# Performance work log

Measured on AMD Instinct MI355X. Metric: run time of the kernel, lower is better.

Reference implementation:

```python
import jax, jax.numpy as jnp
import numpy as np

KAPPA = 1.0
SIGMA = 0.3
EPS = 1e-5  # torch BatchNorm1d default eps


def _bn(y, g, b):
    # training-mode batch norm: biased batch statistics over the batch axis
    mu = jnp.mean(y, axis=0)
    var = jnp.mean((y - mu) ** 2, axis=0)
    return g * (y - mu) * jax.lax.rsqrt(var + EPS) + b


def _hid(x, W, b, g, be):
    # Linear -> BatchNorm1d -> ReLU
    return jax.nn.relu(_bn(x @ W + b, g, be))


def setup_inputs() -> dict:
    key = jax.random.key(0)
    ks = jax.random.split(key, 12)
    B, D, H, T = 2048, 256, 266, 51  # H = dim + 10
    S = T - 1
    sc = jnp.float32(0.1)
    f32 = jnp.float32
    inp = {}
    inp["x"] = jax.random.normal(ks[0], (B, D), f32)
    inp["dW"] = jax.random.normal(ks[1], (S, B, D), f32)   # hoisted per-step noise xi
    inp["law"] = jax.random.normal(ks[2], (S, D), f32)
    inp["timegrid"] = jnp.linspace(0.0, 1.0, T).astype(f32)
    # per-timestep MLP stacks (i_h1 / h1_h2 / h2_o)
    inp["W1"] = sc * jax.random.normal(ks[3], (S, D, H), f32)
    inp["b1"] = jnp.zeros((S, H), f32)
    inp["g1"] = jnp.ones((S, H), f32)
    inp["be1"] = jnp.zeros((S, H), f32)
    inp["W2"] = sc * jax.random.normal(ks[4], (S, H, H), f32)
    inp["b2"] = jnp.zeros((S, H), f32)
    inp["g2"] = jnp.ones((S, H), f32)
    inp["be2"] = jnp.zeros((S, H), f32)
    inp["W3"] = sc * jax.random.normal(ks[5], (S, H, D), f32)
    inp["b3"] = jnp.zeros((S, D), f32)
    # v0 network (v0_i_h1 / v0_h1_h2 / v0_h2_o, all Linear+BN+ReLU)
    inp["Wv1"] = sc * jax.random.normal(ks[6], (D, H), f32)
    inp["bv1"] = jnp.zeros((H,), f32)
    inp["gv1"] = jnp.ones((H,), f32)
    inp["bev1"] = jnp.zeros((H,), f32)
    inp["Wv2"] = sc * jax.random.normal(ks[7], (H, H), f32)
    inp["bv2"] = jnp.zeros((H,), f32)
    inp["gv2"] = jnp.ones((H,), f32)
    inp["bev2"] = jnp.zeros((H,), f32)
    inp["Wv3"] = sc * jax.random.normal(ks[8], (H, 1), f32)
    inp["bv3"] = jnp.zeros((1,), f32)
    inp["gv3"] = jnp.ones((1,), f32)
    inp["bev3"] = jnp.zeros((1,), f32)
    return inp


def reference(x, dW, law, timegrid,
              W1, b1, g1, be1, W2, b2, g2, be2, W3, b3,
              Wv1, bv1, gv1, bev1, Wv2, bv2, gv2, bev2, Wv3, bv3, gv3, bev3):
    hgrid = jnp.diff(timegrid)  # [S]
    # v0 network evaluated on the initial state (note: last stage is also Linear+BN+ReLU)
    v0 = _hid(_hid(_hid(x, Wv1, bv1, gv1, bev1), Wv2, bv2, gv2, bev2), Wv3, bv3, gv3, bev3)  # [B,1]

    def step(carry, xs):
        xc, v = carry
        w1, bb1, gg1, bbe1, w2, bb2, gg2, bbe2, w3, bb3, li, dw, h = xs
        h1 = _hid(xc, w1, bb1, gg1, bbe1)
        h2 = _hid(h1, w2, bb2, gg2, bbe2)
        grad = h2 @ w3 + bb3                                   # [B,D]
        # f = kappa^2/2 * ||x - law_i||^2 + 1/2 * ||alpha||^2,  alpha = -grad
        f = 0.5 * KAPPA ** 2 * jnp.sum((xc - li) ** 2, axis=1) + 0.5 * jnp.sum(grad ** 2, axis=1)
        noise = SIGMA * jnp.sqrt(h) * dw                       # [B,D]
        # diag(grad @ noise^T) == rowwise dot product: O(B*D) instead of O(B^2*D)
        v = v - (f * h)[:, None] + jnp.sum(grad * noise, axis=1, keepdims=True)
        xc = xc - grad * h + noise
        return (xc, v), None

    (x_final, v), _ = jax.lax.scan(
        step, (x, v0),
        (W1, b1, g1, be1, W2, b2, g2, be2, W3, b3, law, dW, hgrid))
    return v  # [B,1]; (x_final and the path are byproducts of the same scan)
```

## Files before the change

kernel.cpp:

```cpp
#include <hip/hip_runtime.h>
#include <hip/hip_bf16.h>


#define BATCH 2048
#define DD    256
#define HH    266
#define HP    272
#define SS    50
#define BN_EPS 1e-5f
#define SIG   0.3f
#define AS_STRIDE 296

#define XC_OFF 0
#define Y1_OFF 524288
#define Y2_OFF 1081344
#define V_OFF  1638400
#define S1_OFF 1640448
#define S2_OFF 1649152
#define S1V_OFF 1657856
#define S2V_OFF 1662208
#define SV_OFF  1666560
#define WQ_OFF  1666576

#define W1S 69632
#define W2S 78336
#define W3S 73728
#define W1Q_OFF 0
#define W2Q_OFF 3481600
#define W3Q_OFF 7398400
#define WV1Q_OFF 11084800
#define WV2Q_OFF 11154432

#define BAR_OFF 7283200

typedef unsigned short ushort_t;
using short8 = __attribute__((ext_vector_type(8))) short;
using f32x4  = __attribute__((ext_vector_type(4))) float;

__device__ __forceinline__ ushort_t f2b(float f) {
    unsigned u = __float_as_uint(f);
    unsigned r = u + 0x7FFF + ((u >> 16) & 1);
    return (ushort_t)(r >> 16);
}

__device__ __forceinline__ float ld_coh(const float* p) {
    return __hip_atomic_load((const float*)p, __ATOMIC_RELAXED, __HIP_MEMORY_SCOPE_AGENT);
}

__device__ __forceinline__ void prefetch16(const void* p, int n16, int tid) {
    const f32x4* q = (const f32x4*)p;
    for (int i = tid; i < n16; i += 512) {
        f32x4 t = q[i];
        asm volatile("" :: "v"(t));
    }
}

__global__ __launch_bounds__(256) void k_conv(const float* __restrict__ src,
                                              ushort_t* __restrict__ dst,
                                              int K, int N, int KT, int NT,
                                              long total) {
    long t = (long)blockIdx.x * 256 + threadIdx.x;
    if (t >= total) return;
    int per = KT * NT * 512;
    int step = (int)(t / per);
    int e = (int)(t - (long)step * per);
    int kt = e / (NT * 512);
    int r = e - kt * NT * 512;
    int nt = r / 512;
    int r2 = r & 511;
    int lane = r2 >> 3;
    int j = r2 & 7;
    int k = kt * 32 + (lane >> 4) * 8 + j;
    int n = nt * 16 + (lane & 15);
    float v = (k < K && n < N) ? src[(size_t)step * K * N + (size_t)k * N + n] : 0.f;
    dst[t] = f2b(v);
}

__global__ __launch_bounds__(256) void k_pre(float* __restrict__ ws) {
    unsigned* bar = (unsigned*)(ws + BAR_OFF);
    for (int i = threadIdx.x; i < 512; i += 256) atomicExch(bar + i, 0u);
}

__device__ __forceinline__ void grid_bar(unsigned* bar, unsigned gen, int bid) {
    __syncthreads();
    if (threadIdx.x == 0) {
        unsigned* leaf = bar + (bid & 7) * 32;
        unsigned* root = bar + 256;
        unsigned* rel  = bar + 288;
        bool done = false;
        unsigned a = __hip_atomic_fetch_add(leaf, 1u, __ATOMIC_RELAXED, __HIP_MEMORY_SCOPE_AGENT);
        if (a == gen * 16u + 15u) {
            unsigned r = __hip_atomic_fetch_add(root, 1u, __ATOMIC_RELAXED, __HIP_MEMORY_SCOPE_AGENT);
            if (r == gen * 8u + 7u) {
                __hip_atomic_store(rel, gen + 1u, __ATOMIC_RELAXED, __HIP_MEMORY_SCOPE_AGENT);
                done = true;
            }
        }
        if (!done) {
            while (__hip_atomic_load(rel, __ATOMIC_RELAXED, __HIP_MEMORY_SCOPE_AGENT) < gen + 1u)
                __builtin_amdgcn_s_sleep(1);
        }
        asm volatile("" ::: "memory");
    }
    __syncthreads();
}

__device__ __forceinline__ void compute_ac_coh(const float* __restrict__ si,
                                               const float* __restrict__ g,
                                               const float* __restrict__ be,
                                               float (*AC)[HP]) {
    int t = threadIdx.x;
    if (t < HP) {
        float a = 0.f, c = 0.f;
        if (t < HH) {
            float s = 0.f, q = 0.f;
            #pragma unroll
            for (int r = 0; r < 8; ++r) {
                s += ld_coh(si + r * 544 + t);
                q += ld_coh(si + r * 544 + 272 + t);
            }
            float mu  = s * (1.0f / 2048.0f);
            float var = q * (1.0f / 2048.0f) - mu * mu;
            float rs  = rsqrtf(fmaxf(var, 0.0f) + BN_EPS);
            a = g[t] * rs;
            c = be[t] - mu * a;
        }
        AC[0][t] = a;
        AC[1][t] = c;
    }
}

__device__ __forceinline__ void dev_lin16(
    int bid, int mode, int KT,
    const float* __restrict__ gsrc,
    const float* __restrict__ lsrc,
    const float* __restrict__ stats_in, const float* __restrict__ g,
    const float* __restrict__ be,
    const ushort_t* __restrict__ Wq, const float* __restrict__ bias,
    float* __restrict__ ylds,
    float* __restrict__ stats_out,
    float* __restrict__ zero_ptr,
    ushort_t* __restrict__ As, float (*AC)[HP])
{
    const int tid  = threadIdx.x;
    const int lane = tid & 63;
    const int wv   = tid >> 6;
    const int quad = lane >> 4;
    const int l15  = lane & 15;
    const int row0 = bid * 16;

    if (zero_ptr != nullptr) {
        int z = bid * 512 + tid;
        if (z < 4352) atomicExch(zero_ptr + z, 0.0f);
    }

    if (mode == 2) { compute_ac_coh(stats_in, g, be, AC); __syncthreads(); }

    const int PAIRS = KT * 16;
    for (int idx = tid; idx < 16 * PAIRS; idx += 512) {
        int m  = idx / PAIRS;
        int kk = (idx - m * PAIRS) * 2;
        float v0, v1;
        if (mode == 2) {
            v0 = (kk < HH)   ? fmaxf(fmaf(AC[0][kk],   lsrc[m * HP + kk],   AC[1][kk]),   0.f) : 0.f;
            v1 = (kk+1 < HH) ? fmaxf(fmaf(AC[0][kk+1], lsrc[m * HP + kk+1], AC[1][kk+1]), 0.f) : 0.f;
        } else {
            v0 = gsrc[(size_t)(row0 + m) * DD + kk];
            v1 = gsrc[(size_t)(row0 + m) * DD + kk + 1];
        }
        ((unsigned int*)As)[m * (AS_STRIDE/2) + (kk >> 1)] =
            (unsigned int)f2b(v0) | ((unsigned int)f2b(v1) << 16);
    }
    __syncthreads();

    f32x4 acc[3];
    #pragma unroll
    for (int i = 0; i < 3; ++i) acc[i] = (f32x4){0.f, 0.f, 0.f, 0.f};

    for (int kt = 0; kt < KT; ++kt) {
        short8 af = *(const short8*)(&As[l15 * AS_STRIDE + kt * 32 + quad * 8]);
        const ushort_t* wp = Wq + ((size_t)(kt * 17 + wv)) * 512 + lane * 8;
        #pragma unroll
        for (int i = 0; i < 3; ++i) {
            if (i < 2 || wv == 0) {
                short8 bf = *(const short8*)(wp + (size_t)i * 8 * 512);
                acc[i] = __builtin_amdgcn_mfma_f32_16x16x32_bf16(af, bf, acc[i], 0, 0, 0);
            }
        }
    }

    #pragma unroll
    for (int i = 0; i < 3; ++i) {
        if (i == 2 && wv != 0) continue;
        int t = wv + 8 * i;
        int col = t * 16 + l15;
        float bj = (col < HH) ? bias[col] : 0.f;
        float y0 = acc[i][0] + bj, y1 = acc[i][1] + bj;
        float y2 = acc[i][2] + bj, y3 = acc[i][3] + bj;
        ylds[(quad*4 + 0) * HP + col] = y0;
        ylds[(quad*4 + 1) * HP + col] = y1;
        ylds[(quad*4 + 2) * HP + col] = y2;
        ylds[(quad*4 + 3) * HP + col] = y3;
        float sp = y0 + y1 + y2 + y3;
        float sq = y0*y0 + y1*y1 + y2*y2 + y3*y3;
        sp += __shfl_xor(sp, 16); sp += __shfl_xor(sp, 32);
        sq += __shfl_xor(sq, 16); sq += __shfl_xor(sq, 32);
        if (quad == 0 && col < HH) {
            float* spp = stats_out + (bid & 7) * 544;
            atomicAdd(spp + col, sp);
            atomicAdd(spp + 272 + col, sq);
        }
    }
}

__device__ __forceinline__ void dev_fused16(
    int bid,
    const float* __restrict__ y2l,
    const float* __restrict__ stats_in,
    const float* __restrict__ g2, const float* __restrict__ be2,
    const ushort_t* __restrict__ W3q, const float* __restrict__ b3,
    const float* __restrict__ law, const float* __restrict__ dWs,
    const float* __restrict__ tg, int s, int doP1,
    float* __restrict__ xcl,
    float* __restrict__ vv, float* __restrict__ outv,
    const ushort_t* __restrict__ W1q, const float* __restrict__ b1n,
    float* __restrict__ y1l,
    float* __restrict__ stats_out,
    float* __restrict__ zero_ptr,
    ushort_t* __restrict__ As, float (*AC)[HP], float* __restrict__ red)
{
    const int tid  = threadIdx.x;
    const int lane = tid & 63;
    const int wv   = tid >> 6;
    const int quad = lane >> 4;
    const int l15  = lane & 15;
    const int row0 = bid * 16;

    if (zero_ptr != nullptr) {
        int z = bid * 512 + tid;
        if (z < 4352) atomicExch(zero_ptr + z, 0.0f);
    }

    compute_ac_coh(stats_in, g2, be2, AC);
    __syncthreads();

    for (int idx = tid; idx < 16 * 144; idx += 512) {
        int m  = idx / 144;
        int kk = (idx - m * 144) * 2;
        float v0 = (kk < HH)   ? fmaxf(fmaf(AC[0][kk],   y2l[m * HP + kk],   AC[1][kk]),   0.f) : 0.f;
        float v1 = (kk+1 < HH) ? fmaxf(fmaf(AC[0][kk+1], y2l[m * HP + kk+1], AC[1][kk+1]), 0.f) : 0.f;
        ((unsigned int*)As)[m * (AS_STRIDE/2) + (kk >> 1)] =
            (unsigned int)f2b(v0) | ((unsigned int)f2b(v1) << 16);
    }
    __syncthreads();

    f32x4 acc[2];
    acc[0] = (f32x4){0.f,0.f,0.f,0.f};
    acc[1] = (f32x4){0.f,0.f,0.f,0.f};
    for (int kt = 0; kt < 9; ++kt) {
        short8 af = *(const short8*)(&As[l15 * AS_STRIDE + kt * 32 + quad * 8]);
        const ushort_t* wp = W3q + ((size_t)(kt * 16 + wv)) * 512 + lane * 8;
        acc[0] = __builtin_amdgcn_mfma_f32_16x16x32_bf16(af, *(const short8*)(wp),           acc[0], 0, 0, 0);
        acc[1] = __builtin_amdgcn_mfma_f32_16x16x32_bf16(af, *(const short8*)(wp + 8 * 512), acc[1], 0, 0, 0);
    }

    const float h   = tg[s + 1] - tg[s];
    const float srt = SIG * sqrtf(h);
    float grad[2][4], xcv[2][4], dwv[2][4];
    float sxr[4] = {0,0,0,0}, sgr[4] = {0,0,0,0}, sgnr[4] = {0,0,0,0};
    #pragma unroll
    for (int i = 0; i < 2; ++i) {
        int col = (wv + 8*i) * 16 + l15;
        #pragma unroll
        for (int r = 0; r < 4; ++r) {
            int rl = quad * 4 + r;
            float gd = acc[i][r] + b3[col];
            float xv = xcl[rl * DD + col];
            float dw = dWs[(size_t)(row0 + rl) * DD + col];
            float d  = xv - law[col];
            grad[i][r] = gd; xcv[i][r] = xv; dwv[i][r] = dw;
            sxr[r]  = fmaf(d, d, sxr[r]);
            sgr[r]  = fmaf(gd, gd, sgr[r]);
            sgnr[r] = fmaf(gd, dw, sgnr[r]);
        }
    }
    #pragma unroll
    for (int off = 1; off < 16; off <<= 1) {
        #pragma unroll
        for (int r = 0; r < 4; ++r) {
            sxr[r]  += __shfl_xor(sxr[r],  off);
            sgr[r]  += __shfl_xor(sgr[r],  off);
            sgnr[r] += __shfl_xor(sgnr[r], off);
        }
    }
    if (l15 == 0) {
        #pragma unroll
        for (int r = 0; r < 4; ++r) {
            int rr = quad * 4 + r;
            red[(wv * 16 + rr) * 3 + 0] = sxr[r];
            red[(wv * 16 + rr) * 3 + 1] = sgr[r];
            red[(wv * 16 + rr) * 3 + 2] = sgnr[r];
        }
    }
    __syncthreads();

    if (tid < 16) {
        float sx = 0.f, sg = 0.f, sgn = 0.f;
        #pragma unroll
        for (int w = 0; w < 8; ++w) {
            sx  += red[(w * 16 + tid) * 3 + 0];
            sg  += red[(w * 16 + tid) * 3 + 1];
            sgn += red[(w * 16 + tid) * 3 + 2];
        }
        int row = row0 + tid;
        float f  = 0.5f * (sx + sg);
        float vn = vv[row] - f * h + srt * sgn;
        vv[row] = vn;
        if (s == SS - 1) outv[row] = vn;
    }

    #pragma unroll
    for (int i = 0; i < 2; ++i) {
        int col = (wv + 8*i) * 16 + l15;
        #pragma unroll
        for (int r = 0; r < 4; ++r) {
            int rl = quad * 4 + r;
            float xn = xcv[i][r] - grad[i][r] * h + srt * dwv[i][r];
            xcl[rl * DD + col] = xn;
            if (doP1) As[rl * AS_STRIDE + col] = f2b(xn);
        }
    }
    if (!doP1) return;
    __syncthreads();

    f32x4 acc2[3];
    #pragma unroll
    for (int i = 0; i < 3; ++i) acc2[i] = (f32x4){0.f, 0.f, 0.f, 0.f};
    for (int kt = 0; kt < 8; ++kt) {
        short8 af = *(const short8*)(&As[l15 * AS_STRIDE + kt * 32 + quad * 8]);
        const ushort_t* wp = W1q + ((size_t)(kt * 17 + wv)) * 512 + lane * 8;
        #pragma unroll
        for (int i = 0; i < 3; ++i) {
            if (i < 2 || wv == 0) {
                short8 bf = *(const short8*)(wp + (size_t)i * 8 * 512);
                acc2[i] = __builtin_amdgcn_mfma_f32_16x16x32_bf16(af, bf, acc2[i], 0, 0, 0);
            }
        }
    }
    #pragma unroll
    for (int i = 0; i < 3; ++i) {
        if (i == 2 && wv != 0) continue;
        int t = wv + 8 * i;
        int col = t * 16 + l15;
        float bj = (col < HH) ? b1n[col] : 0.f;
        float y0 = acc2[i][0] + bj, y1 = acc2[i][1] + bj;
        float y2 = acc2[i][2] + bj, y3 = acc2[i][3] + bj;
        y1l[(quad*4 + 0) * HP + col] = y0;
        y1l[(quad*4 + 1) * HP + col] = y1;
        y1l[(quad*4 + 2) * HP + col] = y2;
        y1l[(quad*4 + 3) * HP + col] = y3;
        float sp = y0 + y1 + y2 + y3;
        float sq = y0*y0 + y1*y1 + y2*y2 + y3*y3;
        sp += __shfl_xor(sp, 16); sp += __shfl_xor(sp, 32);
        sq += __shfl_xor(sq, 16); sq += __shfl_xor(sq, 32);
        if (quad == 0 && col < HH) {
            float* spp = stats_out + (bid & 7) * 544;
            atomicAdd(spp + col, sp);
            atomicAdd(spp + 272 + col, sq);
        }
    }
}

__device__ __forceinline__ void dev_v0l3_16(
    int bid, const float* __restrict__ y2l, const float* __restrict__ stats_in,
    const float* __restrict__ gv, const float* __restrict__ bev,
    const float* __restrict__ wv3, const float* __restrict__ bv3,
    float* __restrict__ vout, float* __restrict__ sv,
    float (*AC)[HP], float* __restrict__ xtra)
{
    const int tid = threadIdx.x;
    compute_ac_coh(stats_in, gv, bev, AC);
    __syncthreads();

    const int r   = tid >> 5;
    const int ks  = tid & 31;
    int k0 = ks * 9, k1 = k0 + 9;
    if (k1 > HH) k1 = HH;
    float acc = 0.0f;
    for (int k = k0; k < k1; ++k) {
        float y  = y2l[r * HP + k];
        float a2 = fmaxf(fmaf(AC[0][k], y, AC[1][k]), 0.0f);
        acc = fmaf(a2, wv3[k], acc);
    }
    #pragma unroll
    for (int off = 1; off < 32; off <<= 1) acc += __shfl_xor(acc, off);
    if (ks == 0) {
        float y = acc + bv3[0];
        vout[bid * 16 + r] = y;
        xtra[r] = y;
        xtra[16 + r] = y * y;
    }
    __syncthreads();
    if (tid == 0) {
        float s = 0.f, q = 0.f;
        #pragma unroll
        for (int i = 0; i < 16; ++i) { s += xtra[i]; q += xtra[16 + i]; }
        atomicAdd(sv, s);
        atomicAdd(sv + 1, q);
    }
}

__device__ __forceinline__ void dev_v0fin16(int bid, float* __restrict__ v,
                                            const float* __restrict__ sv,
                                            const float* __restrict__ gv3,
                                            const float* __restrict__ bev3) {
    if (threadIdx.x < 16) {
        float s0 = ld_coh(sv);
        float s1 = ld_coh(sv + 1);
        float mu  = s0 * (1.0f / 2048.0f);
        float var = s1 * (1.0f / 2048.0f) - mu * mu;
        float rs  = rsqrtf(fmaxf(var, 0.0f) + BN_EPS);
        int row = bid * 16 + threadIdx.x;
        float y = v[row];
        v[row] = fmaxf(gv3[0] * (y - mu) * rs + bev3[0], 0.0f);
    }
}

__global__ __launch_bounds__(512) void k_persist(
    const float* __restrict__ x, const float* __restrict__ dW,
    const float* __restrict__ law, const float* __restrict__ tg,
    const float* __restrict__ b1, const float* __restrict__ g1, const float* __restrict__ be1,
    const float* __restrict__ b2, const float* __restrict__ g2, const float* __restrict__ be2,
    const float* __restrict__ b3,
    const float* __restrict__ bv1, const float* __restrict__ gv1, const float* __restrict__ bev1,
    const float* __restrict__ bv2, const float* __restrict__ gv2, const float* __restrict__ bev2,
    const float* __restrict__ Wv3, const float* __restrict__ bv3,
    const float* __restrict__ gv3, const float* __restrict__ bev3,
    float* __restrict__ ws, float* __restrict__ out)
{
    __shared__ ushort_t As[16 * AS_STRIDE];
    __shared__ float AC[2][HP];
    __shared__ float Y1s[16 * HP];
    __shared__ float Y2s[16 * HP];
    __shared__ float XCs[16 * DD];
    __shared__ float XTRA[384];

    const int bid = blockIdx.x;
    const int tid = threadIdx.x;

    float* V   = ws + V_OFF;
    float* S1  = ws + S1_OFF;
    float* S2  = ws + S2_OFF;
    float* S1v = ws + S1V_OFF;
    float* S2v = ws + S2V_OFF;
    float* SV  = ws + SV_OFF;
    ushort_t* WQ = (ushort_t*)(ws + WQ_OFF);
    ushort_t* W1q  = WQ + W1Q_OFF;
    ushort_t* W2q  = WQ + W2Q_OFF;
    ushort_t* W3q  = WQ + W3Q_OFF;
    ushort_t* Wv1q = WQ + WV1Q_OFF;
    ushort_t* Wv2q = WQ + WV2Q_OFF;
    unsigned* bar  = (unsigned*)(ws + BAR_OFF);

    unsigned gen = 0;
    const int sl = (bid >> 3) & 15;

    for (int i = tid; i < 16 * DD; i += 512)
        XCs[i] = x[(size_t)bid * 16 * DD + i];
    {
        int z = bid * 512 + tid;
        if (z < 26128) atomicExch(S1 + z, 0.0f);
    }
    grid_bar(bar, gen, bid); gen++;

    dev_lin16(bid, 0, 8, x, nullptr, nullptr, nullptr, nullptr,
              Wv1q, bv1, Y1s, S1v, nullptr, As, AC);
    grid_bar(bar, gen, bid); gen++;

    dev_lin16(bid, 2, 9, nullptr, Y1s, S1v, gv1, bev1,
              Wv2q, bv2, Y2s, S2v, nullptr, As, AC);
    grid_bar(bar, gen, bid); gen++;

    dev_v0l3_16(bid, Y2s, S2v, gv2, bev2, Wv3, bv3, V, SV, AC, XTRA);
    grid_bar(bar, gen, bid); gen++;

    dev_v0fin16(bid, V, SV, gv3, bev3);
    dev_lin16(bid, 0, 8, x, nullptr, nullptr, nullptr, nullptr,
              W1q, b1, Y1s, S1, nullptr, As, AC);
    prefetch16((const char*)W2q + sl * 9792, 612, tid);
    grid_bar(bar, gen, bid); gen++;

    for (int s = 0; s < SS; ++s) {
        int p = s & 1;
        dev_lin16(bid, 2, 9, nullptr, Y1s, S1 + p * 4352,
                  g1 + s * HH, be1 + s * HH,
                  W2q + (size_t)s * W2S, b2 + s * HH,
                  Y2s, S2 + p * 4352, S1 + (1 - p) * 4352, As, AC);
        prefetch16(dW + (size_t)s * BATCH * DD + (size_t)bid * 16 * DD, 1024, tid);
        prefetch16((const char*)(W3q + (size_t)s * W3S) + sl * 9216, 576, tid);
        if (s + 1 < SS)
            prefetch16((const char*)(W1q + (size_t)(s + 1) * W1S) + sl * 8704, 544, tid);
        grid_bar(bar, gen, bid); gen++;

        int sn = (s + 1 < SS) ? s + 1 : 0;
        dev_fused16(bid, Y2s, S2 + p * 4352,
                    g2 + s * HH, be2 + s * HH,
                    W3q + (size_t)s * W3S, b3 + s * DD,
                    law + s * DD, dW + (size_t)s * BATCH * DD,
                    tg, s, (s < SS - 1) ? 1 : 0,
                    XCs, V, out,
                    W1q + (size_t)sn * W1S, b1 + sn * HH,
                    Y1s, S1 + ((s + 1) & 1) * 4352,
                    S2 + (1 - p) * 4352, As, AC, XTRA);
        if (s + 1 < SS)
            prefetch16((const char*)(W2q + (size_t)(s + 1) * W2S) + sl * 9792, 612, tid);
        grid_bar(bar, gen, bid); gen++;
    }
}

extern "C" void kernel_launch(void* const* d_in, const int* in_sizes, int n_in,
                              void* d_out, int out_size, void* d_ws, size_t ws_size,
                              hipStream_t stream)
{
    (void)in_sizes; (void)n_in; (void)out_size; (void)ws_size;
    const float* x    = (const float*)d_in[0];
    const float* dW   = (const float*)d_in[1];
    const float* law  = (const float*)d_in[2];
    const float* tg   = (const float*)d_in[3];
    const float* W1   = (const float*)d_in[4];
    const float* b1   = (const float*)d_in[5];
    const float* g1   = (const float*)d_in[6];
    const float* be1  = (const float*)d_in[7];
    const float* W2   = (const float*)d_in[8];
    const float* b2   = (const float*)d_in[9];
    const float* g2   = (const float*)d_in[10];
    const float* be2  = (const float*)d_in[11];
    const float* W3   = (const float*)d_in[12];
    const float* b3   = (const float*)d_in[13];
    const float* Wv1  = (const float*)d_in[14];
    const float* bv1  = (const float*)d_in[15];
    const float* gv1  = (const float*)d_in[16];
    const float* bev1 = (const float*)d_in[17];
    const float* Wv2  = (const float*)d_in[18];
    const float* bv2  = (const float*)d_in[19];
    const float* gv2  = (const float*)d_in[20];
    const float* bev2 = (const float*)d_in[21];
    const float* Wv3  = (const float*)d_in[22];
    const float* bv3  = (const float*)d_in[23];
    const float* gv3  = (const float*)d_in[24];
    const float* bev3 = (const float*)d_in[25];

    float* ws = (float*)d_ws;
    ushort_t* WQ = (ushort_t*)(ws + WQ_OFF);
    ushort_t* W1q  = WQ + W1Q_OFF;
    ushort_t* W2q  = WQ + W2Q_OFF;
    ushort_t* W3q  = WQ + W3Q_OFF;
    ushort_t* Wv1q = WQ + WV1Q_OFF;
    ushort_t* Wv2q = WQ + WV2Q_OFF;
    float* out = (float*)d_out;

    k_pre<<<1, 256, 0, stream>>>(ws);
    k_conv<<<13600, 256, 0, stream>>>(W1,  W1q,  DD, HH, 8, 17, (long)SS * W1S);
    k_conv<<<15300, 256, 0, stream>>>(W2,  W2q,  HH, HH, 9, 17, (long)SS * W2S);
    k_conv<<<14400, 256, 0, stream>>>(W3,  W3q,  HH, DD, 9, 16, (long)SS * W3S);
    k_conv<<<272,   256, 0, stream>>>(Wv1, Wv1q, DD, HH, 8, 17, (long)W1S);
    k_conv<<<306,   256, 0, stream>>>(Wv2, Wv2q, HH, HH, 9, 17, (long)W2S);

    k_persist<<<128, 512, 0, stream>>>(
        x, dW, law, tg,
        b1, g1, be1, b2, g2, be2, b3,
        bv1, gv1, bev1, bv2, gv2, bev2,
        Wv3, bv3, gv3, bev3,
        ws, out);
}
```

Before: 1.319 ms.

## Flatten grid barrier, pad LDS strides, vectorize stats loads, retarget prefetch

Replaces the two-level tree grid barrier with a single flat counter and release flag. Pads the LDS row strides for the Y and XC buffers to cut bank conflicts, and loads BN statistics as dwordx2 with one wait. Drops the separate weight-slice L2 prefetch loops and instead prefetches this block's dW, law and b3 into registers during the lin16 staging. Also adds unroll pragmas on the MFMA k-loops. The flat barrier puts all 128 blocks on one atomic, and dropping the weight prefetch may expose more weight-load latency.

```diff
diff --git a/kernel.cpp b/kernel.cpp
--- a/kernel.cpp
+++ b/kernel.cpp
@@ -10,10 +10,9 @@
 #define BN_EPS 1e-5f
 #define SIG   0.3f
 #define AS_STRIDE 296
-
-#define XC_OFF 0
-#define Y1_OFF 524288
-#define Y2_OFF 1081344
+#define YS    276
+#define XS    260
+
 #define V_OFF  1638400
 #define S1_OFF 1640448
 #define S2_OFF 1649152
@@ -36,6 +35,7 @@
 typedef unsigned short ushort_t;
 using short8 = __attribute__((ext_vector_type(8))) short;
 using f32x4  = __attribute__((ext_vector_type(4))) float;
+using f32x2  = __attribute__((ext_vector_type(2))) float;
 
 __device__ __forceinline__ ushort_t f2b(float f) {
     unsigned u = __float_as_uint(f);
@@ -46,13 +46,10 @@
 __device__ __forceinline__ float ld_coh(const float* p) {
     return __hip_atomic_load((const float*)p, __ATOMIC_RELAXED, __HIP_MEMORY_SCOPE_AGENT);
 }
-
-__device__ __forceinline__ void prefetch16(const void* p, int n16, int tid) {
-    const f32x4* q = (const f32x4*)p;
-    for (int i = tid; i < n16; i += 512) {
-        f32x4 t = q[i];
-        asm volatile("" :: "v"(t));
-    }
+__device__ __forceinline__ f32x2 ld2_coh(const float* p) {
+    f32x2 v;
+    asm volatile("global_load_dwordx2 %0, %1, off sc0 sc1" : "=v"(v) : "v"(p));
+    return v;
 }
 
 __global__ __launch_bounds__(256) void k_conv(const float* __restrict__ src,
@@ -78,25 +75,19 @@
 
 __global__ __launch_bounds__(256) void k_pre(float* __restrict__ ws) {
     unsigned* bar = (unsigned*)(ws + BAR_OFF);
-    for (int i = threadIdx.x; i < 512; i += 256) atomicExch(bar + i, 0u);
+    for (int i = threadIdx.x; i < 768; i += 256) atomicExch(bar + i, 0u);
 }
 
 __device__ __forceinline__ void grid_bar(unsigned* bar, unsigned gen, int bid) {
+    (void)bid;
     __syncthreads();
     if (threadIdx.x == 0) {
-        unsigned* leaf = bar + (bid & 7) * 32;
-        unsigned* root = bar + 256;
-        unsigned* rel  = bar + 288;
-        bool done = false;
-        unsigned a = __hip_atomic_fetch_add(leaf, 1u, __ATOMIC_RELAXED, __HIP_MEMORY_SCOPE_AGENT);
-        if (a == gen * 16u + 15u) {
-            unsigned r = __hip_atomic_fetch_add(root, 1u, __ATOMIC_RELAXED, __HIP_MEMORY_SCOPE_AGENT);
-            if (r == gen * 8u + 7u) {
-                __hip_atomic_store(rel, gen + 1u, __ATOMIC_RELAXED, __HIP_MEMORY_SCOPE_AGENT);
-                done = true;
-            }
-        }
-        if (!done) {
+        unsigned* cnt = bar;
+        unsigned* rel = bar + 32;
+        unsigned a = __hip_atomic_fetch_add(cnt, 1u, __ATOMIC_RELAXED, __HIP_MEMORY_SCOPE_AGENT);
+        if (a == gen * 128u + 127u) {
+            __hip_atomic_store(rel, gen + 1u, __ATOMIC_RELAXED, __HIP_MEMORY_SCOPE_AGENT);
+        } else {
             while (__hip_atomic_load(rel, __ATOMIC_RELAXED, __HIP_MEMORY_SCOPE_AGENT) < gen + 1u)
                 __builtin_amdgcn_s_sleep(1);
         }
@@ -110,36 +101,45 @@
                                                const float* __restrict__ be,
                                                float (*AC)[HP]) {
     int t = threadIdx.x;
-    if (t < HP) {
-        float a = 0.f, c = 0.f;
-        if (t < HH) {
-            float s = 0.f, q = 0.f;
-            #pragma unroll
-            for (int r = 0; r < 8; ++r) {
-                s += ld_coh(si + r * 544 + t);
-                q += ld_coh(si + r * 544 + 272 + t);
+    if (t < 136) {
+        f32x2 sv[8], qv[8];
+        #pragma unroll
+        for (int r = 0; r < 8; ++r) {
+            sv[r] = ld2_coh(si + r * 544 + 2 * t);
+            qv[r] = ld2_coh(si + r * 544 + 272 + 2 * t);
+        }
+        asm volatile("s_waitcnt vmcnt(0)" ::: "memory");
+        __builtin_amdgcn_sched_barrier(0);
+        f32x2 s = sv[0], q = qv[0];
+        #pragma unroll
+        for (int r = 1; r < 8; ++r) { s += sv[r]; q += qv[r]; }
+        #pragma unroll
+        for (int j = 0; j < 2; ++j) {
+            int col = 2 * t + j;
+            float a = 0.f, c = 0.f;
+            if (col < HH) {
+                float mu  = s[j] * (1.0f / 2048.0f);
+                float var = q[j] * (1.0f / 2048.0f) - mu * mu;
+                float rs  = rsqrtf(fmaxf(var, 0.0f) + BN_EPS);
+                a = g[col] * rs;
+                c = be[col] - mu * a;
             }
-            float mu  = s * (1.0f / 2048.0f);
-            float var = q * (1.0f / 2048.0f) - mu * mu;
-            float rs  = rsqrtf(fmaxf(var, 0.0f) + BN_EPS);
-            a = g[t] * rs;
-            c = be[t] - mu * a;
-        }
-        AC[0][t] = a;
-        AC[1][t] = c;
+            AC[0][col] = a;
+            AC[1][col] = c;
+        }
     }
 }
 
 __device__ __forceinline__ void dev_lin16(
     int bid, int mode, int KT,
-    const float* __restrict__ gsrc,
-    const float* __restrict__ lsrc,
+    const float* __restrict__ gsrc, const float* __restrict__ lsrc,
     const float* __restrict__ stats_in, const float* __restrict__ g,
     const float* __restrict__ be,
     const ushort_t* __restrict__ Wq, const float* __restrict__ bias,
-    float* __restrict__ ylds,
-    float* __restrict__ stats_out,
+    float* __restrict__ ylds, float* __restrict__ stats_out,
     float* __restrict__ zero_ptr,
+    const float* __restrict__ pfd, const float* __restrict__ pfl,
+    const float* __restrict__ pfb,
     ushort_t* __restrict__ As, float (*AC)[HP])
 {
     const int tid  = threadIdx.x;
@@ -149,6 +149,14 @@
     const int l15  = lane & 15;
     const int row0 = bid * 16;
 
+    f32x4 pv0 = {0.f,0.f,0.f,0.f}, pv1 = {0.f,0.f,0.f,0.f}, pv2 = {0.f,0.f,0.f,0.f};
+    if (pfd != nullptr) {
+        pv0 = ((const f32x4*)pfd)[tid];
+        pv1 = ((const f32x4*)pfd)[tid + 512];
+        if (tid < 64)        pv2 = ((const f32x4*)pfl)[tid];
+        else if (tid < 128)  pv2 = ((const f32x4*)pfb)[tid - 64];
+    }
+
     if (zero_ptr != nullptr) {
         int z = bid * 512 + tid;
         if (z < 4352) atomicExch(zero_ptr + z, 0.0f);
@@ -162,8 +170,8 @@
         int kk = (idx - m * PAIRS) * 2;
         float v0, v1;
         if (mode == 2) {
-            v0 = (kk < HH)   ? fmaxf(fmaf(AC[0][kk],   lsrc[m * HP + kk],   AC[1][kk]),   0.f) : 0.f;
-            v1 = (kk+1 < HH) ? fmaxf(fmaf(AC[0][kk+1], lsrc[m * HP + kk+1], AC[1][kk+1]), 0.f) : 0.f;
+            v0 = (kk < HH)   ? fmaxf(fmaf(AC[0][kk],   lsrc[m * YS + kk],   AC[1][kk]),   0.f) : 0.f;
+            v1 = (kk+1 < HH) ? fmaxf(fmaf(AC[0][kk+1], lsrc[m * YS + kk+1], AC[1][kk+1]), 0.f) : 0.f;
         } else {
             v0 = gsrc[(size_t)(row0 + m) * DD + kk];
             v1 = gsrc[(size_t)(row0 + m) * DD + kk + 1];
@@ -171,12 +179,17 @@
         ((unsigned int*)As)[m * (AS_STRIDE/2) + (kk >> 1)] =
             (unsigned int)f2b(v0) | ((unsigned int)f2b(v1) << 16);
     }
+    if (pfd != nullptr) {
+        asm volatile("" :: "v"(pv0), "v"(pv1));
+        if (tid < 128) asm volatile("" :: "v"(pv2));
+    }
     __syncthreads();
 
     f32x4 acc[3];
     #pragma unroll
     for (int i = 0; i < 3; ++i) acc[i] = (f32x4){0.f, 0.f, 0.f, 0.f};
 
+    #pragma unroll 3
     for (int kt = 0; kt < KT; ++kt) {
         short8 af = *(const short8*)(&As[l15 * AS_STRIDE + kt * 32 + quad * 8]);
         const ushort_t* wp = Wq + ((size_t)(kt * 17 + wv)) * 512 + lane * 8;
@@ -197,10 +210,10 @@
         float bj = (col < HH) ? bias[col] : 0.f;
         float y0 = acc[i][0] + bj, y1 = acc[i][1] + bj;
         float y2 = acc[i][2] + bj, y3 = acc[i][3] + bj;
-        ylds[(quad*4 + 0) * HP + col] = y0;
-        ylds[(quad*4 + 1) * HP + col] = y1;
-        ylds[(quad*4 + 2) * HP + col] = y2;
-        ylds[(quad*4 + 3) * HP + col] = y3;
+        ylds[(quad*4 + 0) * YS + col] = y0;
+        ylds[(quad*4 + 1) * YS + col] = y1;
+        ylds[(quad*4 + 2) * YS + col] = y2;
+        ylds[(quad*4 + 3) * YS + col] = y3;
         float sp = y0 + y1 + y2 + y3;
         float sq = y0*y0 + y1*y1 + y2*y2 + y3*y3;
         sp += __shfl_xor(sp, 16); sp += __shfl_xor(sp, 32);
@@ -215,17 +228,14 @@
 
 __device__ __forceinline__ void dev_fused16(
     int bid,
-    const float* __restrict__ y2l,
-    const float* __restrict__ stats_in,
+    const float* __restrict__ y2l, const float* __restrict__ stats_in,
     const float* __restrict__ g2, const float* __restrict__ be2,
     const ushort_t* __restrict__ W3q, const float* __restrict__ b3,
     const float* __restrict__ law, const float* __restrict__ dWs,
     const float* __restrict__ tg, int s, int doP1,
-    float* __restrict__ xcl,
-    float* __restrict__ vv, float* __restrict__ outv,
+    float* __restrict__ xcl, float* __restrict__ vv, float* __restrict__ outv,
     const ushort_t* __restrict__ W1q, const float* __restrict__ b1n,
-    float* __restrict__ y1l,
-    float* __restrict__ stats_out,
+    float* __restrict__ y1l, float* __restrict__ stats_out,
     float* __restrict__ zero_ptr,
     ushort_t* __restrict__ As, float (*AC)[HP], float* __restrict__ red)
 {
@@ -247,8 +257,8 @@
     for (int idx = tid; idx < 16 * 144; idx += 512) {
         int m  = idx / 144;
         int kk = (idx - m * 144) * 2;
-        float v0 = (kk < HH)   ? fmaxf(fmaf(AC[0][kk],   y2l[m * HP + kk],   AC[1][kk]),   0.f) : 0.f;
-        float v1 = (kk+1 < HH) ? fmaxf(fmaf(AC[0][kk+1], y2l[m * HP + kk+1], AC[1][kk+1]), 0.f) : 0.f;
+        float v0 = (kk < HH)   ? fmaxf(fmaf(AC[0][kk],   y2l[m * YS + kk],   AC[1][kk]),   0.f) : 0.f;
+        float v1 = (kk+1 < HH) ? fmaxf(fmaf(AC[0][kk+1], y2l[m * YS + kk+1], AC[1][kk+1]), 0.f) : 0.f;
         ((unsigned int*)As)[m * (AS_STRIDE/2) + (kk >> 1)] =
             (unsigned int)f2b(v0) | ((unsigned int)f2b(v1) << 16);
     }
@@ -257,6 +267,7 @@
     f32x4 acc[2];
     acc[0] = (f32x4){0.f,0.f,0.f,0.f};
     acc[1] = (f32x4){0.f,0.f,0.f,0.f};
+    #pragma unroll 3
     for (int kt = 0; kt < 9; ++kt) {
         short8 af = *(const short8*)(&As[l15 * AS_STRIDE + kt * 32 + quad * 8]);
         const ushort_t* wp = W3q + ((size_t)(kt * 16 + wv)) * 512 + lane * 8;
@@ -267,21 +278,29 @@
     const float h   = tg[s + 1] - tg[s];
     const float srt = SIG * sqrtf(h);
     float grad[2][4], xcv[2][4], dwv[2][4];
-    float sxr[4] = {0,0,0,0}, sgr[4] = {0,0,0,0}, sgnr[4] = {0,0,0,0};
+    float sxr[4], sgr[4], sgnr[4];
     #pragma unroll
     for (int i = 0; i < 2; ++i) {
         int col = (wv + 8*i) * 16 + l15;
+        const float lawv = law[col];
+        const float b3v  = b3[col];
         #pragma unroll
         for (int r = 0; r < 4; ++r) {
             int rl = quad * 4 + r;
-            float gd = acc[i][r] + b3[col];
-            float xv = xcl[rl * DD + col];
+            float gd = acc[i][r] + b3v;
+            float xv = xcl[rl * XS + col];
             float dw = dWs[(size_t)(row0 + rl) * DD + col];
-            float d  = xv - law[col];
+            float d  = xv - lawv;
             grad[i][r] = gd; xcv[i][r] = xv; dwv[i][r] = dw;
-            sxr[r]  = fmaf(d, d, sxr[r]);
-            sgr[r]  = fmaf(gd, gd, sgr[r]);
-            sgnr[r] = fmaf(gd, dw, sgnr[r]);
+            if (i == 0) {
+                sxr[r]  = d * d;
+                sgr[r]  = gd * gd;
+                sgnr[r] = gd * dw;
+            } else {
+                sxr[r]  = fmaf(d, d, sxr[r]);
+                sgr[r]  = fmaf(gd, gd, sgr[r]);
+                sgnr[r] = fmaf(gd, dw, sgnr[r]);
+            }
         }
     }
     #pragma unroll
@@ -326,7 +345,7 @@
         for (int r = 0; r < 4; ++r) {
             int rl = quad * 4 + r;
             float xn = xcv[i][r] - grad[i][r] * h + srt * dwv[i][r];
-            xcl[rl * DD + col] = xn;
+            xcl[rl * XS + col] = xn;
             if (doP1) As[rl * AS_STRIDE + col] = f2b(xn);
         }
     }
@@ -336,6 +355,7 @@
     f32x4 acc2[3];
     #pragma unroll
     for (int i = 0; i < 3; ++i) acc2[i] = (f32x4){0.f, 0.f, 0.f, 0.f};
+    #pragma unroll 4
     for (int kt = 0; kt < 8; ++kt) {
         short8 af = *(const short8*)(&As[l15 * AS_STRIDE + kt * 32 + quad * 8]);
         const ushort_t* wp = W1q + ((size_t)(kt * 17 + wv)) * 512 + lane * 8;
@@ -355,10 +375,10 @@
         float bj = (col < HH) ? b1n[col] : 0.f;
         float y0 = acc2[i][0] + bj, y1 = acc2[i][1] + bj;
         float y2 = acc2[i][2] + bj, y3 = acc2[i][3] + bj;
-        y1l[(quad*4 + 0) * HP + col] = y0;
-        y1l[(quad*4 + 1) * HP + col] = y1;
-        y1l[(quad*4 + 2) * HP + col] = y2;
-        y1l[(quad*4 + 3) * HP + col] = y3;
+        y1l[(quad*4 + 0) * YS + col] = y0;
+        y1l[(quad*4 + 1) * YS + col] = y1;
+        y1l[(quad*4 + 2) * YS + col] = y2;
+        y1l[(quad*4 + 3) * YS + col] = y3;
         float sp = y0 + y1 + y2 + y3;
         float sq = y0*y0 + y1*y1 + y2*y2 + y3*y3;
         sp += __shfl_xor(sp, 16); sp += __shfl_xor(sp, 32);
@@ -382,13 +402,13 @@
     compute_ac_coh(stats_in, gv, bev, AC);
     __syncthreads();
 
-    const int r   = tid >> 5;
-    const int ks  = tid & 31;
+    const int r  = tid >> 5;
+    const int ks = tid & 31;
     int k0 = ks * 9, k1 = k0 + 9;
     if (k1 > HH) k1 = HH;
     float acc = 0.0f;
     for (int k = k0; k < k1; ++k) {
-        float y  = y2l[r * HP + k];
+        float y  = y2l[r * YS + k];
         float a2 = fmaxf(fmaf(AC[0][k], y, AC[1][k]), 0.0f);
         acc = fmaf(a2, wv3[k], acc);
     }
@@ -440,9 +460,9 @@
 {
     __shared__ ushort_t As[16 * AS_STRIDE];
     __shared__ float AC[2][HP];
-    __shared__ float Y1s[16 * HP];
-    __shared__ float Y2s[16 * HP];
-    __shared__ float XCs[16 * DD];
+    __shared__ float Y1s[16 * YS];
+    __shared__ float Y2s[16 * YS];
+    __shared__ float XCs[16 * XS];
     __shared__ float XTRA[384];
 
     const int bid = blockIdx.x;
@@ -463,10 +483,11 @@
     unsigned* bar  = (unsigned*)(ws + BAR_OFF);
 
     unsigned gen = 0;
-    const int sl = (bid >> 3) & 15;
-
-    for (int i = tid; i < 16 * DD; i += 512)
-        XCs[i] = x[(size_t)bid * 16 * DD + i];
+
+    for (int i = tid; i < 16 * DD; i += 512) {
+        int r = i >> 8, c = i & 255;
+        XCs[r * XS + c] = x[(size_t)bid * 16 * DD + i];
+    }
     {
         int z = bid * 512 + tid;
         if (z < 26128) atomicExch(S1 + z, 0.0f);
@@ -474,11 +495,11 @@
     grid_bar(bar, gen, bid); gen++;
 
     dev_lin16(bid, 0, 8, x, nullptr, nullptr, nullptr, nullptr,
-              Wv1q, bv1, Y1s, S1v, nullptr, As, AC);
+              Wv1q, bv1, Y1s, S1v, nullptr, nullptr, nullptr, nullptr, As, AC);
     grid_bar(bar, gen, bid); gen++;
 
     dev_lin16(bid, 2, 9, nullptr, Y1s, S1v, gv1, bev1,
-              Wv2q, bv2, Y2s, S2v, nullptr, As, AC);
+              Wv2q, bv2, Y2s, S2v, nullptr, nullptr, nullptr, nullptr, As, AC);
     grid_bar(bar, gen, bid); gen++;
 
     dev_v0l3_16(bid, Y2s, S2v, gv2, bev2, Wv3, bv3, V, SV, AC, XTRA);
@@ -486,8 +507,7 @@
 
     dev_v0fin16(bid, V, SV, gv3, bev3);
     dev_lin16(bid, 0, 8, x, nullptr, nullptr, nullptr, nullptr,
-              W1q, b1, Y1s, S1, nullptr, As, AC);
-    prefetch16((const char*)W2q + sl * 9792, 612, tid);
+              W1q, b1, Y1s, S1, nullptr, nullptr, nullptr, nullptr, As, AC);
     grid_bar(bar, gen, bid); gen++;
 
     for (int s = 0; s < SS; ++s) {
@@ -495,11 +515,9 @@
         dev_lin16(bid, 2, 9, nullptr, Y1s, S1 + p * 4352,
                   g1 + s * HH, be1 + s * HH,
                   W2q + (size_t)s * W2S, b2 + s * HH,
-                  Y2s, S2 + p * 4352, S1 + (1 - p) * 4352, As, AC);
-        prefetch16(dW + (size_t)s * BATCH * DD + (size_t)bid * 16 * DD, 1024, tid);
-        prefetch16((const char*)(W3q + (size_t)s * W3S) + sl * 9216, 576, tid);
-        if (s + 1 < SS)
-            prefetch16((const char*)(W1q + (size_t)(s + 1) * W1S) + sl * 8704, 544, tid);
+                  Y2s, S2 + p * 4352, S1 + (1 - p) * 4352,
+                  dW + (size_t)s * BATCH * DD + (size_t)bid * 16 * DD,
+                  law + (size_t)s * DD, b3 + (size_t)s * DD, As, AC);
         grid_bar(bar, gen, bid); gen++;
 
         int sn = (s + 1 < SS) ? s + 1 : 0;
@@ -512,8 +530,6 @@
                     W1q + (size_t)sn * W1S, b1 + sn * HH,
                     Y1s, S1 + ((s + 1) & 1) * 4352,
                     S2 + (1 - p) * 4352, As, AC, XTRA);
-        if (s + 1 < SS)
-            prefetch16((const char*)(W2q + (size_t)(s + 1) * W2S) + sl * 9792, 612, tid);
         grid_bar(bar, gen, bid); gen++;
     }
 }
```

Measured after the change: 1.458 ms. 1.11x slower.
